# Kernel optimization log

Hardware: AMD Instinct MI355X
Metric: run time of the kernel (lower is better)

The kernel has to match this reference:

```python
import jax, jax.numpy as jnp
import numpy as np

B, N, INP = 16, 1024, 256
HEADS, DIM_HEAD = 8, 32
INNER = HEADS * DIM_HEAD  # 256
OUP = 256
IH = IW = 32  # IH*IW == N


def _relative_index(ih, iw):
    # mirrors the torch __init__ construction (meshgrid indexing='ij')
    coords = np.stack(np.meshgrid(np.arange(ih), np.arange(iw), indexing='ij')).reshape(2, -1)
    rel = coords[:, :, None] - coords[:, None, :]  # [2, N, N]
    rel[0] += ih - 1
    rel[1] += iw - 1
    rel[0] *= 2 * iw - 1
    return rel.sum(0).reshape(-1)  # [N*N]


def setup_inputs() -> dict:
    key = jax.random.key(0)
    kx, kqkv, kout, kbias = jax.random.split(key, 4)
    x = jax.random.normal(kx, (B, N, INP), dtype=jnp.float32)
    w_qkv = jax.random.normal(kqkv, (INP, 3 * INNER), dtype=jnp.float32) * 0.02
    w_out = jax.random.normal(kout, (INNER, OUP), dtype=jnp.float32) * 0.02
    b_out = jnp.zeros((OUP,), dtype=jnp.float32)
    bias_table = jax.random.normal(kbias, ((2 * IH - 1) * (2 * IW - 1), HEADS), dtype=jnp.float32) * 0.02
    relative_index = jnp.asarray(_relative_index(IH, IW), dtype=jnp.int32)
    return {"x": x, "w_qkv": w_qkv, "w_out": w_out, "b_out": b_out,
            "bias_table": bias_table, "relative_index": relative_index}


def reference(x, w_qkv, w_out, b_out, bias_table, relative_index):
    b, n, _ = x.shape
    scale = DIM_HEAD ** (-0.5)
    qkv = x @ w_qkv  # [b, n, 3*inner]
    q, k, v = jnp.split(qkv, 3, axis=-1)
    split_heads = lambda t: t.reshape(b, n, HEADS, DIM_HEAD).transpose(0, 2, 1, 3)  # b h n d
    q, k, v = split_heads(q), split_heads(k), split_heads(v)
    dots = jnp.einsum('bhnd,bhmd->bhnm', q, k) * scale  # [b, h, n, n]
    # gather bias: (n*n, heads) -> (1, heads, n, n), matching '(h w) c -> 1 c h w'
    rel_bias = bias_table[relative_index].reshape(n, n, HEADS).transpose(2, 0, 1)[None]
    attn = jax.nn.softmax(dots + rel_bias, axis=-1)
    out = jnp.einsum('bhnm,bhmd->bhnd', attn, v)
    out = out.transpose(0, 2, 1, 3).reshape(b, n, INNER)  # b n (h d)
    return out @ w_out + b_out
```

## Files before the change

kernel.cpp:

```cpp
#include <hip/hip_runtime.h>
#include <hip/hip_bf16.h>

typedef __bf16 bf16;
typedef bf16 bf16x4 __attribute__((ext_vector_type(4)));
typedef bf16 bf16x8 __attribute__((ext_vector_type(8)));
typedef short s16x4 __attribute__((ext_vector_type(4)));
typedef float f32x4 __attribute__((ext_vector_type(4)));

#define MFMA32(A, B, C) __builtin_amdgcn_mfma_f32_16x16x32_bf16(A, B, C, 0, 0, 0)
#define MFMA16(A, B, C) __builtin_amdgcn_mfma_f32_16x16x16bf16_1k(A, B, C, 0, 0, 0)
#define GL2LDS16(gp, lp)                                                            \
  __builtin_amdgcn_global_load_lds((const __attribute__((address_space(1))) unsigned int*)(gp), \
                                   (__attribute__((address_space(3))) unsigned int*)(lp), 16, 0, 0)

static constexpr float SCALE = 0.17677669529663687f;
static constexpr float LOG2E = 1.4426950408889634f;

__global__ __launch_bounds__(256) void k_prep(const float* __restrict__ x,
                                              const float* __restrict__ wqkv,
                                              const float* __restrict__ wout,
                                              const float* __restrict__ table,
                                              const int* __restrict__ ridx,
                                              bf16* __restrict__ xb, bf16* __restrict__ wtq,
                                              bf16* __restrict__ wto, bf16* __restrict__ rbb) {
  const int tid = threadIdx.x;
  const int blk = blockIdx.x;
  if (blk < 2048) {
    int t = blk * 256 + tid;
    const float4* s = reinterpret_cast<const float4*>(x) + (size_t)t * 2;
    float4 a = s[0], c = s[1];
    bf16x8 o;
    o[0] = (bf16)a.x; o[1] = (bf16)a.y; o[2] = (bf16)a.z; o[3] = (bf16)a.w;
    o[4] = (bf16)c.x; o[5] = (bf16)c.y; o[6] = (bf16)c.z; o[7] = (bf16)c.w;
    reinterpret_cast<bf16x8*>(xb)[t] = o;
  } else if (blk < 3072) {
    int t = (blk - 2048) * 256 + tid;
    if (t < 196608) {
      int n = t >> 8, k = t & 255;
      wtq[t] = (bf16)wqkv[k * 768 + n];
    } else {
      int t2 = t - 196608;
      int n = t2 >> 8, k = t2 & 255;
      wto[t2] = (bf16)wout[k * 256 + n];
    }
  } else {
    const int bb2 = blk - 3072;
    const int qt = bb2 >> 6, kt = bb2 & 63;
    const int r = tid & 3, lane = tid >> 2;
    const int ln = lane & 15, quad = lane >> 4;
    const int qrow = qt * 16 + ln;
    const int key = kt * 16 + quad * 4 + r;
    const int idx = ridx[qrow * 1024 + key];
    const float4* p = reinterpret_cast<const float4*>(table) + idx * 2;
    float4 a = p[0], c = p[1];
    float vals[8] = {a.x, a.y, a.z, a.w, c.x, c.y, c.z, c.w};
    const int base = bb2 * 256 + tid;
#pragma unroll
    for (int h = 0; h < 8; ++h) rbb[h * 1048576 + base] = (bf16)(vals[h] * LOG2E);
  }
}

template <int EPI>
__global__ __launch_bounds__(256) void k_gemm(const bf16* __restrict__ A,
                                              const bf16* __restrict__ Bt,
                                              bf16* __restrict__ q, bf16* __restrict__ kk,
                                              bf16* __restrict__ vt, float* __restrict__ out,
                                              const float* __restrict__ bout) {
  __shared__ __align__(16) bf16 As[2][4096];
  __shared__ __align__(16) bf16 Bs[2][4096];
  const int tid = threadIdx.x;
  const int ln = tid & 15, quad = (tid >> 4) & 3, wv = tid >> 6;
  const int wm = (wv >> 1) * 64, wn = (wv & 1) * 64;
  const int m0 = blockIdx.x * 128, n0 = blockIdx.y * 128;
  const int srow = tid >> 2, scg = (tid & 3) * 8;
  const bf16* ag = A + (size_t)(m0 + srow) * 256 + scg;
  const bf16* bg = Bt + (size_t)(n0 + srow) * 256 + scg;
  f32x4 acc[4][4] = {};

  GL2LDS16(ag, &As[0][tid * 8]);
  GL2LDS16(ag + 64 * 256, &As[0][2048 + tid * 8]);
  GL2LDS16(bg, &Bs[0][tid * 8]);
  GL2LDS16(bg + 64 * 256, &Bs[0][2048 + tid * 8]);

#pragma unroll 2
  for (int kt = 0; kt < 256; kt += 32) {
    const int cur = (kt >> 5) & 1, nxt = cur ^ 1;
    __syncthreads();
    if (kt < 224) {
      GL2LDS16(ag + kt + 32, &As[nxt][tid * 8]);
      GL2LDS16(ag + 64 * 256 + kt + 32, &As[nxt][2048 + tid * 8]);
      GL2LDS16(bg + kt + 32, &Bs[nxt][tid * 8]);
      GL2LDS16(bg + 64 * 256 + kt + 32, &Bs[nxt][2048 + tid * 8]);
    }
    bf16x8 af[4], bfr[4];
#pragma unroll
    for (int i = 0; i < 4; ++i)
      af[i] = *reinterpret_cast<const bf16x8*>(&As[cur][(wm + i * 16 + ln) * 32 + quad * 8]);
#pragma unroll
    for (int i = 0; i < 4; ++i)
      bfr[i] = *reinterpret_cast<const bf16x8*>(&Bs[cur][(wn + i * 16 + ln) * 32 + quad * 8]);
#pragma unroll
    for (int i = 0; i < 4; ++i)
#pragma unroll
      for (int j = 0; j < 4; ++j) acc[i][j] = MFMA32(af[i], bfr[j], acc[i][j]);
  }

  if (EPI == 0) {
    const int colbase = n0 + wn;
    const int seg = colbase >> 8;
    const int cb = colbase & 255;
    const float mul = (seg == 0) ? SCALE * LOG2E : 1.0f;
#pragma unroll
    for (int i = 0; i < 4; ++i) {
      const int gm = m0 + wm + i * 16 + quad * 4;
      const int b = gm >> 10;
#pragma unroll
      for (int j = 0; j < 4; ++j) {
        const int gc = cb + j * 16 + ln;
        const int h = gc >> 5, d = gc & 31;
#pragma unroll
        for (int r = 0; r < 4; ++r) {
          const int nseq = (gm + r) & 1023;
          if (seg == 2) {
            vt[(b * 8 + h) * 32768 + d * 1024 + nseq] = (bf16)acc[i][j][r];
          } else {
            bf16* dst = (seg == 0) ? q : kk;
            dst[(b * 8 + h) * 32768 + nseq * 32 + d] = (bf16)(acc[i][j][r] * mul);
          }
        }
      }
    }
  } else {
#pragma unroll
    for (int j = 0; j < 4; ++j) {
      const int gc = n0 + wn + j * 16 + ln;
      const float bb = bout[gc];
#pragma unroll
      for (int i = 0; i < 4; ++i) {
        const int gm = m0 + wm + i * 16 + quad * 4;
#pragma unroll
        for (int r = 0; r < 4; ++r) out[(size_t)(gm + r) * 256 + gc] = acc[i][j][r] + bb;
      }
    }
  }
}

__global__ __launch_bounds__(256, 6) void k_flash(const bf16* __restrict__ qs,
                                                  const bf16* __restrict__ ks,
                                                  const bf16* __restrict__ vtg,
                                                  const bf16* __restrict__ rbb,
                                                  bf16* __restrict__ ao) {
  __shared__ __align__(16) bf16 Ks[2][2048];
  __shared__ __align__(16) bf16 Vs[2][2048];
  const int tid = threadIdx.x;
  const int lane = tid & 63;
  const int ln = lane & 15, quad = lane >> 4, wv = tid >> 6;
  const int blk = blockIdx.x;
  const int bh = blk & 127;
  const int b = bh >> 3, h = bh & 7;
  const int qtw = (blk >> 7) * 4 + wv;
  const int q0 = qtw * 16;
  const bf16* qb = qs + bh * 32768;
  const bf16* kb = ks + bh * 32768;
  const bf16* vb = vtg + bh * 32768;
  const bf16* bbias = rbb + h * 1048576 + qtw * 16384 + lane * 4;

  const bf16* kg = kb + (tid >> 2) * 32 + (((tid & 3) ^ ((tid >> 3) & 3)) * 8);
  const bf16* vg = vb + (tid >> 3) * 1024 + (((tid & 7) ^ ((tid >> 3) & 7)) * 8);

  const bf16x8 qfrag = *reinterpret_cast<const bf16x8*>(&qb[(q0 + ln) * 32 + quad * 8]);

  const int ksw = (quad ^ ((ln >> 1) & 3)) * 8;
  const int vswl = ln & 7;

  f32x4 acc0 = {0.f, 0.f, 0.f, 0.f}, acc1 = {0.f, 0.f, 0.f, 0.f};
  float lsum = 0.f;

  bf16x4 cbf[2][4];
#pragma unroll
  for (int nt = 0; nt < 4; ++nt) cbf[0][nt] = *reinterpret_cast<const bf16x4*>(&bbias[nt * 256]);
  GL2LDS16(kg, &Ks[0][tid * 8]);
  GL2LDS16(vg, &Vs[0][tid * 8]);

#pragma unroll 2
  for (int it = 0; it < 16; ++it) {
    const int cur = it & 1, nxt = cur ^ 1;
    const int k0 = it * 64;
    __syncthreads();
    if (it < 15) {
      GL2LDS16(kg + (k0 + 64) * 32, &Ks[nxt][tid * 8]);
      GL2LDS16(vg + k0 + 64, &Vs[nxt][tid * 8]);
#pragma unroll
      for (int nt = 0; nt < 4; ++nt)
        cbf[nxt][nt] = *reinterpret_cast<const bf16x4*>(&bbias[((it + 1) * 4 + nt) * 256]);
    }
    bf16x8 kf[4];
#pragma unroll
    for (int nt = 0; nt < 4; ++nt)
      kf[nt] = *reinterpret_cast<const bf16x8*>(&Ks[cur][(nt * 16 + ln) * 32 + ksw]);
    s16x4 vfa[4], vfc[4];
#pragma unroll
    for (int nt = 0; nt < 4; ++nt) {
      const int col = ((2 * nt + (quad >> 1)) ^ vswl) * 8 + (quad & 1) * 4;
      vfa[nt] = *reinterpret_cast<const s16x4*>(&Vs[cur][ln * 64 + col]);
      vfc[nt] = *reinterpret_cast<const s16x4*>(&Vs[cur][(ln + 16) * 64 + col]);
    }
    f32x4 s[4];
#pragma unroll
    for (int nt = 0; nt < 4; ++nt) {
      f32x4 c;
#pragma unroll
      for (int e = 0; e < 4; ++e) c[e] = (float)cbf[cur][nt][e];
      s[nt] = MFMA32(kf[nt], qfrag, c);
    }
    s16x4 p[4];
#pragma unroll
    for (int nt = 0; nt < 4; ++nt) {
      bf16x4 t;
#pragma unroll
      for (int e = 0; e < 4; ++e) {
        s[nt][e] = __builtin_amdgcn_exp2f(s[nt][e]);
        t[e] = (bf16)s[nt][e];
      }
      lsum += (s[nt][0] + s[nt][1]) + (s[nt][2] + s[nt][3]);
      p[nt] = __builtin_bit_cast(s16x4, t);
    }
    acc0 = MFMA16(p[0], vfa[0], acc0);
    acc1 = MFMA16(p[0], vfc[0], acc1);
    acc0 = MFMA16(p[1], vfa[1], acc0);
    acc1 = MFMA16(p[1], vfc[1], acc1);
    acc0 = MFMA16(p[2], vfa[2], acc0);
    acc1 = MFMA16(p[2], vfc[2], acc1);
    acc0 = MFMA16(p[3], vfa[3], acc0);
    acc1 = MFMA16(p[3], vfc[3], acc1);
  }
  __syncthreads();

  lsum += __shfl_xor(lsum, 16, 64);
  lsum += __shfl_xor(lsum, 32, 64);

#pragma unroll
  for (int r = 0; r < 4; ++r) {
    const float inv = __builtin_amdgcn_rcpf(__shfl(lsum, quad * 4 + r, 64));
    const int row = q0 + quad * 4 + r;
    bf16* po = &ao[(size_t)(b * 1024 + row) * 256 + h * 32 + ln];
    po[0] = (bf16)(acc0[r] * inv);
    po[16] = (bf16)(acc1[r] * inv);
  }
}

extern "C" void kernel_launch(void* const* d_in, const int* in_sizes, int n_in,
                              void* d_out, int out_size, void* d_ws, size_t ws_size,
                              hipStream_t stream) {
  const float* x = (const float*)d_in[0];
  const float* wqkv = (const float*)d_in[1];
  const float* wout = (const float*)d_in[2];
  const float* bout = (const float*)d_in[3];
  const float* btab = (const float*)d_in[4];
  const int* ridx = (const int*)d_in[5];
  float* out = (float*)d_out;

  char* ws = (char*)d_ws;
  bf16* xb  = (bf16*)(ws + 0);
  bf16* wtq = (bf16*)(ws + 8388608);
  bf16* wto = (bf16*)(ws + 8781824);
  bf16* q   = (bf16*)(ws + 8912896);
  bf16* k   = (bf16*)(ws + 17301504);
  bf16* vt  = (bf16*)(ws + 25690112);
  bf16* rb  = (bf16*)(ws + 34078720);
  bf16* ao  = (bf16*)(ws + 50855936);

  k_prep<<<7168, 256, 0, stream>>>(x, wqkv, wout, btab, ridx, xb, wtq, wto, rb);
  k_gemm<0><<<dim3(128, 6), 256, 0, stream>>>(xb, wtq, q, k, vt, nullptr, nullptr);
  k_flash<<<2048, 256, 0, stream>>>(q, k, vt, rb, ao);
  k_gemm<1><<<dim3(128, 2), 256, 0, stream>>>(ao, wto, nullptr, nullptr, nullptr, out, bout);
}
```

Baseline: 151.9 us.

## Process two 16-row query tiles per wave in flash attention kernel

Each wave now computes 32 query rows instead of 16, reusing the same K and V fragments loaded from LDS for both row tiles. The grid is halved and the occupancy hint lowered from 6 to 4 to make room for the doubled accumulators and bias buffers. This cuts LDS reads and block overhead per unit of work, at the cost of more registers, fewer resident waves and less parallelism to hide latency.

```diff
diff --git a/kernel.cpp b/kernel.cpp
--- a/kernel.cpp
+++ b/kernel.cpp
@@ -145,7 +145,7 @@
   }
 }
 
-__global__ __launch_bounds__(256, 6) void k_flash(const bf16* __restrict__ qs,
+__global__ __launch_bounds__(256, 4) void k_flash(const bf16* __restrict__ qs,
                                                   const bf16* __restrict__ ks,
                                                   const bf16* __restrict__ vtg,
                                                   const bf16* __restrict__ rbb,
@@ -159,26 +159,32 @@
   const int bh = blk & 127;
   const int b = bh >> 3, h = bh & 7;
   const int qtw = (blk >> 7) * 4 + wv;
-  const int q0 = qtw * 16;
+  const int q0 = qtw * 32;
   const bf16* qb = qs + bh * 32768;
   const bf16* kb = ks + bh * 32768;
   const bf16* vb = vtg + bh * 32768;
-  const bf16* bbias = rbb + h * 1048576 + qtw * 16384 + lane * 4;
+  const bf16* bbias0 = rbb + h * 1048576 + (2 * qtw) * 16384 + lane * 4;
+  const bf16* bbias1 = bbias0 + 16384;
 
   const bf16* kg = kb + (tid >> 2) * 32 + (((tid & 3) ^ ((tid >> 3) & 3)) * 8);
   const bf16* vg = vb + (tid >> 3) * 1024 + (((tid & 7) ^ ((tid >> 3) & 7)) * 8);
 
-  const bf16x8 qfrag = *reinterpret_cast<const bf16x8*>(&qb[(q0 + ln) * 32 + quad * 8]);
+  const bf16x8 qfrag0 = *reinterpret_cast<const bf16x8*>(&qb[(q0 + ln) * 32 + quad * 8]);
+  const bf16x8 qfrag1 = *reinterpret_cast<const bf16x8*>(&qb[(q0 + 16 + ln) * 32 + quad * 8]);
 
   const int ksw = (quad ^ ((ln >> 1) & 3)) * 8;
   const int vswl = ln & 7;
 
-  f32x4 acc0 = {0.f, 0.f, 0.f, 0.f}, acc1 = {0.f, 0.f, 0.f, 0.f};
-  float lsum = 0.f;
-
-  bf16x4 cbf[2][4];
-#pragma unroll
-  for (int nt = 0; nt < 4; ++nt) cbf[0][nt] = *reinterpret_cast<const bf16x4*>(&bbias[nt * 256]);
+  f32x4 a00 = {0.f, 0.f, 0.f, 0.f}, a01 = {0.f, 0.f, 0.f, 0.f};
+  f32x4 a10 = {0.f, 0.f, 0.f, 0.f}, a11 = {0.f, 0.f, 0.f, 0.f};
+  float lsum0 = 0.f, lsum1 = 0.f;
+
+  bf16x4 cbf[2][2][4];
+#pragma unroll
+  for (int nt = 0; nt < 4; ++nt) {
+    cbf[0][0][nt] = *reinterpret_cast<const bf16x4*>(&bbias0[nt * 256]);
+    cbf[0][1][nt] = *reinterpret_cast<const bf16x4*>(&bbias1[nt * 256]);
+  }
   GL2LDS16(kg, &Ks[0][tid * 8]);
   GL2LDS16(vg, &Vs[0][tid * 8]);
 
@@ -191,8 +197,10 @@
       GL2LDS16(kg + (k0 + 64) * 32, &Ks[nxt][tid * 8]);
       GL2LDS16(vg + k0 + 64, &Vs[nxt][tid * 8]);
 #pragma unroll
-      for (int nt = 0; nt < 4; ++nt)
-        cbf[nxt][nt] = *reinterpret_cast<const bf16x4*>(&bbias[((it + 1) * 4 + nt) * 256]);
+      for (int nt = 0; nt < 4; ++nt) {
+        cbf[nxt][0][nt] = *reinterpret_cast<const bf16x4*>(&bbias0[((it + 1) * 4 + nt) * 256]);
+        cbf[nxt][1][nt] = *reinterpret_cast<const bf16x4*>(&bbias1[((it + 1) * 4 + nt) * 256]);
+      }
     }
     bf16x8 kf[4];
 #pragma unroll
@@ -205,47 +213,61 @@
       vfa[nt] = *reinterpret_cast<const s16x4*>(&Vs[cur][ln * 64 + col]);
       vfc[nt] = *reinterpret_cast<const s16x4*>(&Vs[cur][(ln + 16) * 64 + col]);
     }
-    f32x4 s[4];
-#pragma unroll
-    for (int nt = 0; nt < 4; ++nt) {
-      f32x4 c;
-#pragma unroll
-      for (int e = 0; e < 4; ++e) c[e] = (float)cbf[cur][nt][e];
-      s[nt] = MFMA32(kf[nt], qfrag, c);
-    }
-    s16x4 p[4];
-#pragma unroll
-    for (int nt = 0; nt < 4; ++nt) {
-      bf16x4 t;
+    f32x4 s0[4], s1[4];
+#pragma unroll
+    for (int nt = 0; nt < 4; ++nt) {
+      f32x4 c0, c1;
 #pragma unroll
       for (int e = 0; e < 4; ++e) {
-        s[nt][e] = __builtin_amdgcn_exp2f(s[nt][e]);
-        t[e] = (bf16)s[nt][e];
-      }
-      lsum += (s[nt][0] + s[nt][1]) + (s[nt][2] + s[nt][3]);
-      p[nt] = __builtin_bit_cast(s16x4, t);
-    }
-    acc0 = MFMA16(p[0], vfa[0], acc0);
-    acc1 = MFMA16(p[0], vfc[0], acc1);
-    acc0 = MFMA16(p[1], vfa[1], acc0);
-    acc1 = MFMA16(p[1], vfc[1], acc1);
-    acc0 = MFMA16(p[2], vfa[2], acc0);
-    acc1 = MFMA16(p[2], vfc[2], acc1);
-    acc0 = MFMA16(p[3], vfa[3], acc0);
-    acc1 = MFMA16(p[3], vfc[3], acc1);
+        c0[e] = (float)cbf[cur][0][nt][e];
+        c1[e] = (float)cbf[cur][1][nt][e];
+      }
+      s0[nt] = MFMA32(kf[nt], qfrag0, c0);
+      s1[nt] = MFMA32(kf[nt], qfrag1, c1);
+    }
+    s16x4 p0[4], p1[4];
+#pragma unroll
+    for (int nt = 0; nt < 4; ++nt) {
+      bf16x4 t0, t1;
+#pragma unroll
+      for (int e = 0; e < 4; ++e) {
+        s0[nt][e] = __builtin_amdgcn_exp2f(s0[nt][e]);
+        t0[e] = (bf16)s0[nt][e];
+        s1[nt][e] = __builtin_amdgcn_exp2f(s1[nt][e]);
+        t1[e] = (bf16)s1[nt][e];
+      }
+      lsum0 += (s0[nt][0] + s0[nt][1]) + (s0[nt][2] + s0[nt][3]);
+      lsum1 += (s1[nt][0] + s1[nt][1]) + (s1[nt][2] + s1[nt][3]);
+      p0[nt] = __builtin_bit_cast(s16x4, t0);
+      p1[nt] = __builtin_bit_cast(s16x4, t1);
+    }
+#pragma unroll
+    for (int nt = 0; nt < 4; ++nt) {
+      a00 = MFMA16(p0[nt], vfa[nt], a00);
+      a01 = MFMA16(p0[nt], vfc[nt], a01);
+      a10 = MFMA16(p1[nt], vfa[nt], a10);
+      a11 = MFMA16(p1[nt], vfc[nt], a11);
+    }
   }
   __syncthreads();
 
-  lsum += __shfl_xor(lsum, 16, 64);
-  lsum += __shfl_xor(lsum, 32, 64);
+  lsum0 += __shfl_xor(lsum0, 16, 64);
+  lsum0 += __shfl_xor(lsum0, 32, 64);
+  lsum1 += __shfl_xor(lsum1, 16, 64);
+  lsum1 += __shfl_xor(lsum1, 32, 64);
 
 #pragma unroll
   for (int r = 0; r < 4; ++r) {
-    const float inv = __builtin_amdgcn_rcpf(__shfl(lsum, quad * 4 + r, 64));
-    const int row = q0 + quad * 4 + r;
-    bf16* po = &ao[(size_t)(b * 1024 + row) * 256 + h * 32 + ln];
-    po[0] = (bf16)(acc0[r] * inv);
-    po[16] = (bf16)(acc1[r] * inv);
+    const float inv0 = __builtin_amdgcn_rcpf(__shfl(lsum0, quad * 4 + r, 64));
+    const int row0 = q0 + quad * 4 + r;
+    bf16* po0 = &ao[(size_t)(b * 1024 + row0) * 256 + h * 32 + ln];
+    po0[0] = (bf16)(a00[r] * inv0);
+    po0[16] = (bf16)(a01[r] * inv0);
+    const float inv1 = __builtin_amdgcn_rcpf(__shfl(lsum1, quad * 4 + r, 64));
+    const int row1 = q0 + 16 + quad * 4 + r;
+    bf16* po1 = &ao[(size_t)(b * 1024 + row1) * 256 + h * 32 + ln];
+    po1[0] = (bf16)(a10[r] * inv1);
+    po1[16] = (bf16)(a11[r] * inv1);
   }
 }
 
@@ -272,6 +294,6 @@
 
   k_prep<<<7168, 256, 0, stream>>>(x, wqkv, wout, btab, ridx, xb, wtq, wto, rb);
   k_gemm<0><<<dim3(128, 6), 256, 0, stream>>>(xb, wtq, q, k, vt, nullptr, nullptr);
-  k_flash<<<2048, 256, 0, stream>>>(q, k, vt, rb, ao);
+  k_flash<<<1024, 256, 0, stream>>>(q, k, vt, rb, ao);
   k_gemm<1><<<dim3(128, 2), 256, 0, stream>>>(ao, wto, nullptr, nullptr, nullptr, out, bout);
 }
```

Result: no change. 150.1 us (-1.2%).
